# Kernel tuning notes

Measured on AMD Instinct MI355X. Metric: run time of the kernel, lower is better.

## Reference

```python
import jax, jax.numpy as jnp
import numpy as np

IN_DIM, OUT_DIM, N_PROTO, RANK = 1024, 1024, 32, 16


def setup_inputs() -> dict:
    key = jax.random.key(0)
    ks = jax.random.split(key, 5)
    x = jax.random.normal(ks[0], (2, 4096, IN_DIM), dtype=jnp.float32)
    prototypes = jax.random.normal(ks[1], (N_PROTO, IN_DIM), dtype=jnp.float32) * 0.02
    B = jax.random.normal(ks[2], (N_PROTO, RANK, IN_DIM), dtype=jnp.float32) * 0.02
    A = jax.random.normal(ks[3], (N_PROTO, OUT_DIM, RANK), dtype=jnp.float32) * 0.02
    bias = jnp.zeros((N_PROTO, OUT_DIM), dtype=jnp.float32)
    temp = jnp.asarray(1.0, dtype=jnp.float32)
    return {"x": x, "prototypes": prototypes, "B": B, "A": A, "bias": bias, "temp": temp}


def reference(x, prototypes, B, A, bias, temp):
    lead = x.shape[:-1]
    xf = x.reshape(-1, IN_DIM)                       # [N, in]
    x2 = jnp.sum(xf * xf, axis=1, keepdims=True)     # [N,1]
    p2 = jnp.sum(prototypes * prototypes, axis=1)    # [P]
    d2 = x2 + p2[None, :] - 2.0 * (xf @ prototypes.T)
    dists = jnp.sqrt(jnp.maximum(d2, 0.0))           # [N,P]
    t = jnp.maximum(jnp.abs(temp), 0.1)
    w = jax.nn.softmax(-dists / t, axis=1)           # [N,P]
    topw, topi = jax.lax.top_k(w, 2)                 # [N,2]
    topw = topw / jnp.sum(topw, axis=1, keepdims=True)
    out = jnp.zeros((xf.shape[0], OUT_DIM), dtype=xf.dtype)
    for tslot in range(2):
        idx = topi[:, tslot]                          # [N]
        wt = topw[:, tslot:tslot + 1]                 # [N,1]
        h = jnp.einsum('nri,ni->nr', B[idx], xf)      # gathered low-rank down-proj
        y = jnp.einsum('nor,nr->no', A[idx], h) + bias[idx]
        out = out + wt * y
    return out.reshape(*lead, OUT_DIM)
```

## Files before the change

kernel.cpp:

```cpp
#include <hip/hip_runtime.h>
#include <math.h>

#define ROWS_TOTAL 8192
#define KDIM 1024
#define NPROTO 32
#define RNK 16
#define OUTD 1024
#define TIE_EPS 1.30e-4
#define DELTA 4.0e-5f
#define FLAG_CAP 4096

__global__ __launch_bounds__(256) void prep_kernel(
    const float* __restrict__ A, const float* __restrict__ B,
    const float* __restrict__ proto, float* __restrict__ At,
    float* __restrict__ Bt, float* __restrict__ Pt, double* __restrict__ p2g,
    int* __restrict__ counts, int* __restrict__ flagcnt)
{
    __shared__ float T[16 * 68];
    __shared__ float U[64 * 20];
    __shared__ double red[32][9];
    __shared__ float TP[32][33];
    const int tid = threadIdx.x;

    if (blockIdx.x < 128) {
        const int p = blockIdx.x >> 2;
        const int c0 = (blockIdx.x & 3) * 4;
        const float4* B4 = (const float4*)(B + (size_t)p * RNK * KDIM);
        const float4* A4 = (const float4*)(A + (size_t)p * OUTD * RNK);
        float4* Bt4 = (float4*)(Bt + (size_t)p * KDIM * RNK);
        float4* At4 = (float4*)(At + (size_t)p * RNK * OUTD);
        for (int c = c0; c < c0 + 4; ++c) {
            {
                int r = tid >> 4, kk = tid & 15;
                float4 v = B4[r * 256 + c * 16 + kk];
                *(float4*)&T[r * 68 + kk * 4] = v;
            }
            {
                int o = tid >> 2, rq = tid & 3;
                float4 v = A4[(c * 64 + o) * 4 + rq];
                *(float4*)&U[o * 20 + rq * 4] = v;
            }
            __syncthreads();
            {
                int k = tid >> 2, rq = tid & 3;
                float4 g = make_float4(T[(rq * 4 + 0) * 68 + k], T[(rq * 4 + 1) * 68 + k],
                                       T[(rq * 4 + 2) * 68 + k], T[(rq * 4 + 3) * 68 + k]);
                Bt4[(c * 64 + k) * 4 + rq] = g;
            }
            {
                int r = tid >> 4, ow = tid & 15;
                float4 g = make_float4(U[(ow * 4 + 0) * 20 + r], U[(ow * 4 + 1) * 20 + r],
                                       U[(ow * 4 + 2) * 20 + r], U[(ow * 4 + 3) * 20 + r]);
                At4[r * 256 + c * 16 + ow] = g;
            }
            __syncthreads();
        }
    } else {
        const int qb = blockIdx.x - 128;
        if (qb == 0) {
            if (tid < 64) counts[tid] = 0;
            if (tid == 64) flagcnt[0] = 0;
            {
                const int p = tid >> 3, seg = tid & 7;
                const float* a = proto + (size_t)p * KDIM + seg * 128;
                double s = 0.0;
                for (int k = 0; k < 128; ++k) {
                    double v = (double)a[k];
                    s = fma(v, v, s);
                }
                red[p][seg] = s;
            }
            __syncthreads();
            if (tid < 32) {
                double acc = red[tid][0];
                #pragma unroll
                for (int j = 1; j < 8; ++j) acc += red[tid][j];
                p2g[tid] = acc;
            }
        }
        float4* Pt4 = (float4*)Pt;
        for (int kc = qb * 8; kc < qb * 8 + 8; ++kc) {
            {
                int cc = tid >> 3, kk4 = tid & 7;
                float4 v = *(const float4*)(proto + (size_t)cc * KDIM + kc * 32 + kk4 * 4);
                TP[cc][kk4 * 4 + 0] = v.x; TP[cc][kk4 * 4 + 1] = v.y;
                TP[cc][kk4 * 4 + 2] = v.z; TP[cc][kk4 * 4 + 3] = v.w;
            }
            __syncthreads();
            {
                int kk = tid >> 3, c4 = tid & 7;
                float4 g = make_float4(TP[c4 * 4 + 0][kk], TP[c4 * 4 + 1][kk],
                                       TP[c4 * 4 + 2][kk], TP[c4 * 4 + 3][kk]);
                Pt4[(kc * 32 + kk) * 8 + c4] = g;
            }
            __syncthreads();
        }
    }
}

#define INS(kb, ib) { \
    bool lt1 = (kb) < k1, lt2 = (kb) < k2, lt3 = (kb) < k3, lt4 = (kb) < k4; \
    float nk4 = lt3 ? k3 : (lt4 ? (kb) : k4); int ni4 = lt3 ? i3 : (lt4 ? (ib) : i4); \
    float nk3 = lt2 ? k2 : (lt3 ? (kb) : k3); int ni3 = lt2 ? i2 : (lt3 ? (ib) : i3); \
    float nk2 = lt1 ? k1 : (lt2 ? (kb) : k2); int ni2 = lt1 ? i1 : (lt2 ? (ib) : i2); \
    k4 = nk4; i4 = ni4; k3 = nk3; i3 = ni3; k2 = nk2; i2 = ni2; \
    if (lt1) { k1 = (kb); i1 = (ib); } }

__global__ __launch_bounds__(256) void route_kernel(
    const float* __restrict__ x, const float* __restrict__ Pt,
    const float* __restrict__ temp, const double* __restrict__ p2g,
    float4* __restrict__ route, int* __restrict__ counts,
    int* __restrict__ flagcnt, int* __restrict__ flaglist)
{
    __shared__ float Xs[8 * KDIM];
    __shared__ float part[4][8][33];
    __shared__ float x2p[4][8];
    __shared__ int lcnt[64];

    const int tid = threadIdx.x;
    const int w = tid >> 6, l = tid & 63;
    const int c4 = l & 7, kslot = l >> 3;
    const int rowbase = blockIdx.x * 8;

    if (tid < 64) lcnt[tid] = 0;

    const float4* x4 = (const float4*)x;
    float sq[8];
    #pragma unroll
    for (int j = 0; j < 8; ++j) {
        float4 v = x4[(size_t)rowbase * 256 + j * 256 + tid];
        ((float4*)Xs)[j * 256 + tid] = v;
        sq[j] = fmaf(v.x, v.x, fmaf(v.y, v.y, fmaf(v.z, v.z, v.w * v.w)));
    }
    #pragma unroll
    for (int m = 1; m < 64; m <<= 1) {
        #pragma unroll
        for (int j = 0; j < 8; ++j) sq[j] += __shfl_xor(sq[j], m);
    }
    if (l == 0) {
        #pragma unroll
        for (int j = 0; j < 8; ++j) x2p[w][j] = sq[j];
    }
    __syncthreads();

    float acc[8][4];
    #pragma unroll
    for (int j = 0; j < 8; ++j)
        #pragma unroll
        for (int jj = 0; jj < 4; ++jj) acc[j][jj] = 0.f;

    const float4* Pt4 = (const float4*)Pt;
    const int kbase = w * 256;
    #pragma unroll 4
    for (int i = 0; i < 32; ++i) {
        const int k = kbase + i * 8 + kslot;
        float4 pv = Pt4[k * 8 + c4];
        #pragma unroll
        for (int j = 0; j < 8; ++j) {
            float xv = Xs[j * KDIM + k];
            acc[j][0] = fmaf(xv, pv.x, acc[j][0]);
            acc[j][1] = fmaf(xv, pv.y, acc[j][1]);
            acc[j][2] = fmaf(xv, pv.z, acc[j][2]);
            acc[j][3] = fmaf(xv, pv.w, acc[j][3]);
        }
    }
    #pragma unroll
    for (int m = 8; m < 64; m <<= 1) {
        #pragma unroll
        for (int j = 0; j < 8; ++j) {
            acc[j][0] += __shfl_xor(acc[j][0], m);
            acc[j][1] += __shfl_xor(acc[j][1], m);
            acc[j][2] += __shfl_xor(acc[j][2], m);
            acc[j][3] += __shfl_xor(acc[j][3], m);
        }
    }
    if (kslot == 0) {
        #pragma unroll
        for (int j = 0; j < 8; ++j) {
            part[w][j][4 * c4 + 0] = acc[j][0];
            part[w][j][4 * c4 + 1] = acc[j][1];
            part[w][j][4 * c4 + 2] = acc[j][2];
            part[w][j][4 * c4 + 3] = acc[j][3];
        }
    }
    __syncthreads();

    {
        const int rowsel = tid >> 5, c = tid & 31;
        float dsum = (part[0][rowsel][c] + part[1][rowsel][c])
                   + (part[2][rowsel][c] + part[3][rowsel][c]);
        float key = (float)(p2g[c] - 2.0 * (double)dsum);
        float x2 = (x2p[0][rowsel] + x2p[1][rowsel])
                 + (x2p[2][rowsel] + x2p[3][rowsel]);

        float k1 = key, k2 = 3.0e38f, k3 = 3.1e38f, k4 = 3.2e38f;
        int i1 = c, i2 = 64, i3 = 65, i4 = 66;
        #pragma unroll
        for (int m = 1; m < 32; m <<= 1) {
            float b1 = __shfl_xor(k1, m), b2 = __shfl_xor(k2, m);
            float b3 = __shfl_xor(k3, m), b4 = __shfl_xor(k4, m);
            int j1 = __shfl_xor(i1, m), j2 = __shfl_xor(i2, m);
            int j3 = __shfl_xor(i3, m), j4 = __shfl_xor(i4, m);
            INS(b1, j1); INS(b2, j2); INS(b3, j3); INS(b4, j4);
        }
        if (c == 0) {
            const int row = rowbase + rowsel;
            const float tf = fmaxf(fabsf(temp[0]), 0.1f);
            bool amb = (k2 - k1 < DELTA) || (k3 - k2 < DELTA)
                    || (fabsf((k3 - k2) - (float)TIE_EPS) < DELTA)
                    || (k4 - k3 < DELTA);
            bool tie = (k3 - k2) < (float)TIE_EPS;
            bool take3 = tie && (i3 < i2);
            float ksel = take3 ? k3 : k2;
            int   isel = take3 ? i3 : i2;
            float d0 = sqrtf(fmaxf(x2 + k1, 0.f));
            float d1 = sqrtf(fmaxf(x2 + ksel, 0.f));
            float e = expf((d0 - d1) / tf);
            float w0 = 1.f / (1.f + e);
            route[row] = make_float4(__int_as_float(i1), __int_as_float(isel),
                                     w0, e * w0);
            atomicAdd(&lcnt[i1], 1);
            atomicAdd(&lcnt[32 + isel], 1);
            if (amb) {
                int fi = atomicAdd(flagcnt, 1);
                if (fi < FLAG_CAP) flaglist[fi] = row;
            }
        }
    }
    __syncthreads();
    if (tid < 64) atomicAdd(&counts[tid], lcnt[tid]);
}

__global__ __launch_bounds__(256) void refine_scan_kernel(
    const float* __restrict__ x, const float* __restrict__ proto,
    const float* __restrict__ temp, const double* __restrict__ p2g,
    float4* __restrict__ route, int* __restrict__ counts,
    const int* __restrict__ flagcnt, const int* __restrict__ flaglist,
    int2* __restrict__ segs)
{
    const int tid = threadIdx.x;
    const int w = tid >> 6, l = tid & 63;
    const int c = l & 31, half = l >> 5;
    const int n = min(flagcnt[0], FLAG_CAP);

    for (int f = w; f < n; f += 4) {
        const int row = flaglist[f];
        const float* xr = x + (size_t)row * KDIM;
        double xs = 0.0;
        for (int k = l * 16; k < l * 16 + 16; ++k) {
            double v = (double)xr[k];
            xs = fma(v, v, xs);
        }
        #pragma unroll
        for (int m = 1; m < 64; m <<= 1) xs += __shfl_xor(xs, m);
        const float* pr = proto + (size_t)c * KDIM + half * 512;
        const float* xh = xr + half * 512;
        double d0a = 0.0, d1a = 0.0;
        for (int k = 0; k < 512; k += 2) {
            d0a = fma((double)xh[k], (double)pr[k], d0a);
            d1a = fma((double)xh[k + 1], (double)pr[k + 1], d1a);
        }
        double acc = d0a + d1a;
        acc += __shfl_xor(acc, 32);
        double key = p2g[c] - 2.0 * acc;

        double k1 = key, k2 = 1.0e300, k3 = 1.1e300;
        int i1 = c, i2 = 64, i3 = 65;
        #pragma unroll
        for (int m = 1; m < 32; m <<= 1) {
            double b1 = __shfl_xor(k1, m), b2 = __shfl_xor(k2, m), b3 = __shfl_xor(k3, m);
            int j1 = __shfl_xor(i1, m), j2 = __shfl_xor(i2, m), j3 = __shfl_xor(i3, m);
            bool c1 = (k1 < b1) || (k1 == b1 && i1 < j1);
            double m1 = c1 ? k1 : b1, M1 = c1 ? b1 : k1;
            int mi1 = c1 ? i1 : j1, Mi1 = c1 ? j1 : i1;
            bool c2 = (k2 < b2) || (k2 == b2 && i2 < j2);
            double m2 = c2 ? k2 : b2;
            int mi2 = c2 ? i2 : j2;
            bool c3 = (k3 < b3) || (k3 == b3 && i3 < j3);
            double m3 = c3 ? k3 : b3;
            int mi3 = c3 ? i3 : j3;
            bool c4 = (M1 < m2) || (M1 == m2 && Mi1 < mi2);
            double t2 = c4 ? M1 : m2, T2 = c4 ? m2 : M1;
            int ti2 = c4 ? Mi1 : mi2, Ti2 = c4 ? mi2 : Mi1;
            bool c5 = (T2 < m3) || (T2 == m3 && Ti2 < mi3);
            k1 = m1; i1 = mi1;
            k2 = t2; i2 = ti2;
            k3 = c5 ? T2 : m3; i3 = c5 ? Ti2 : mi3;
        }
        if (l == 0) {
            const double tmp = (double)fmaxf(fabsf(temp[0]), 0.1f);
            bool tie = (k3 - k2) < TIE_EPS;
            bool take3 = tie && (i3 < i2);
            double ksel = take3 ? k3 : k2;
            int isel = take3 ? i3 : i2;
            double dd0 = sqrt(fmax(xs + k1, 0.0));
            double dd1 = sqrt(fmax(xs + ksel, 0.0));
            float e = expf((float)((dd0 - dd1) / tmp));
            float w0 = 1.f / (1.f + e);
            float4 old = route[row];
            int oi1 = __float_as_int(old.x), oisel = __float_as_int(old.y);
            if (oi1 != i1) { atomicAdd(&counts[oi1], -1); atomicAdd(&counts[i1], 1); }
            if (oisel != isel) { atomicAdd(&counts[32 + oisel], -1); atomicAdd(&counts[32 + isel], 1); }
            route[row] = make_float4(__int_as_float(i1), __int_as_float(isel),
                                     w0, e * w0);
        }
    }
    __syncthreads();
    if (tid < 64) {
        int v = atomicAdd(&counts[tid], 0);
        int sum = v;
        #pragma unroll
        for (int off = 1; off < 32; off <<= 1) {
            int u = __shfl_up(sum, off, 32);
            if ((tid & 31) >= off) sum += u;
        }
        counts[tid] = sum - v;
        segs[tid] = make_int2(sum - v, sum);
    }
}

__global__ __launch_bounds__(256) void scatter_kernel(
    const float4* __restrict__ route, int* __restrict__ counts,
    int* __restrict__ rowlist0, int* __restrict__ rowlist1)
{
    __shared__ int lcnt[64];
    __shared__ int gbase[64];
    const int tid = threadIdx.x;
    const int i = blockIdx.x * 256 + tid;
    if (tid < 64) lcnt[tid] = 0;
    __syncthreads();
    float4 rt = route[i];
    int p0 = __float_as_int(rt.x);
    int p1 = __float_as_int(rt.y);
    int lp0 = atomicAdd(&lcnt[p0], 1);
    int lp1 = atomicAdd(&lcnt[32 + p1], 1);
    __syncthreads();
    if (tid < 64) gbase[tid] = atomicAdd(&counts[tid], lcnt[tid]);
    __syncthreads();
    rowlist0[gbase[p0] + lp0] = i;
    rowlist1[gbase[32 + p1] + lp1] = i;
}

__global__ __launch_bounds__(256) void h_kernel(
    const float* __restrict__ x, const float* __restrict__ Bt,
    const int* __restrict__ rowlist0, const int* __restrict__ rowlist1,
    const int2* __restrict__ segs, float* __restrict__ hws)
{
    __shared__ float part[4][4][17];
    __shared__ int xoffs[4];

    const int tid = threadIdx.x;
    const int w = tid >> 6, l = tid & 63;
    const int kq = l >> 2, rq = l & 3;
    const int s = blockIdx.y;
    const int slot = s >> 5;
    const int2 sg = segs[s];
    const int* rl = slot ? rowlist1 : rowlist0;
    const float4* Btp = (const float4*)(Bt + (size_t)(s & 31) * KDIM * RNK);
    const int qbase = w * 256;

    for (int c = blockIdx.x; ; c += gridDim.x) {
        const int base = sg.x + c * 4;
        if (base >= sg.y) break;
        const int m = min(4, sg.y - base);

        if (tid < 4) xoffs[tid] = rl[base + min(tid, m - 1)] * KDIM;
        __syncthreads();
        const int x0 = xoffs[0], x1 = xoffs[1], x2 = xoffs[2], x3 = xoffs[3];

        float4 a0 = {0,0,0,0}, a1 = {0,0,0,0}, a2 = {0,0,0,0}, a3 = {0,0,0,0};
        #pragma unroll
        for (int i = 0; i < 16; ++i) {
            const int k = qbase + i * 16 + kq;
            float4 bv = Btp[k * 4 + rq];
            float v0 = x[x0 + k], v1 = x[x1 + k], v2 = x[x2 + k], v3 = x[x3 + k];
            a0.x = fmaf(v0, bv.x, a0.x); a0.y = fmaf(v0, bv.y, a0.y);
            a0.z = fmaf(v0, bv.z, a0.z); a0.w = fmaf(v0, bv.w, a0.w);
            a1.x = fmaf(v1, bv.x, a1.x); a1.y = fmaf(v1, bv.y, a1.y);
            a1.z = fmaf(v1, bv.z, a1.z); a1.w = fmaf(v1, bv.w, a1.w);
            a2.x = fmaf(v2, bv.x, a2.x); a2.y = fmaf(v2, bv.y, a2.y);
            a2.z = fmaf(v2, bv.z, a2.z); a2.w = fmaf(v2, bv.w, a2.w);
            a3.x = fmaf(v3, bv.x, a3.x); a3.y = fmaf(v3, bv.y, a3.y);
            a3.z = fmaf(v3, bv.z, a3.z); a3.w = fmaf(v3, bv.w, a3.w);
        }
        #pragma unroll
        for (int msk = 4; msk < 64; msk <<= 1) {
            a0.x += __shfl_xor(a0.x, msk); a0.y += __shfl_xor(a0.y, msk);
            a0.z += __shfl_xor(a0.z, msk); a0.w += __shfl_xor(a0.w, msk);
            a1.x += __shfl_xor(a1.x, msk); a1.y += __shfl_xor(a1.y, msk);
            a1.z += __shfl_xor(a1.z, msk); a1.w += __shfl_xor(a1.w, msk);
            a2.x += __shfl_xor(a2.x, msk); a2.y += __shfl_xor(a2.y, msk);
            a2.z += __shfl_xor(a2.z, msk); a2.w += __shfl_xor(a2.w, msk);
            a3.x += __shfl_xor(a3.x, msk); a3.y += __shfl_xor(a3.y, msk);
            a3.z += __shfl_xor(a3.z, msk); a3.w += __shfl_xor(a3.w, msk);
        }
        if (kq == 0) {
            *(float4*)&part[w][0][rq * 4] = a0;
            *(float4*)&part[w][1][rq * 4] = a1;
            *(float4*)&part[w][2][rq * 4] = a2;
            *(float4*)&part[w][3][rq * 4] = a3;
        }
        __syncthreads();
        if (tid < 64) {
            const int e = tid >> 4, r = tid & 15;
            if (e < m) {
                float hsum = (part[0][e][r] + part[1][e][r])
                           + (part[2][e][r] + part[3][e][r]);
                hws[(size_t)(slot * ROWS_TOTAL + base + e) * 16 + r] = hsum;
            }
        }
        __syncthreads();
    }
}

__global__ __launch_bounds__(256) void y_kernel(
    const float* __restrict__ At, const float* __restrict__ bias,
    const float4* __restrict__ route, const int* __restrict__ rowlist,
    const int2* __restrict__ segs, const float* __restrict__ hws,
    float* __restrict__ out, int slot)
{
    __shared__ float hsm[16][17];
    __shared__ int rows[16];
    __shared__ float wts[16];

    const int tid = threadIdx.x;
    const int f4 = tid;
    const int p = blockIdx.y;
    const int2 sg = segs[slot * 32 + p];
    const float4* Atp = (const float4*)(At + (size_t)p * RNK * OUTD);
    const float4 bb = ((const float4*)(bias + (size_t)p * OUTD))[f4];

    float4 Areg[16];
    #pragma unroll
    for (int r = 0; r < 16; ++r) Areg[r] = Atp[r * 256 + f4];

    for (int c = blockIdx.x; ; c += gridDim.x) {
        const int base = sg.x + c * 16;
        if (base >= sg.y) break;
        const int m = min(16, sg.y - base);
        const int gbase = slot * ROWS_TOTAL + base;

        if (tid < 16) {
            int rr = rowlist[base + min(tid, m - 1)];
            rows[tid] = rr;
            float4 rt = route[rr];
            wts[tid] = slot ? rt.w : rt.z;
        }
        {
            const int e = tid >> 4, r = tid & 15;
            hsm[e][r] = hws[(size_t)(gbase + min(e, m - 1)) * 16 + r];
        }
        __syncthreads();

        for (int e = 0; e < m; ++e) {
            float4 acc = bb;
            #pragma unroll
            for (int r = 0; r < 16; ++r) {
                float hr = hsm[e][r];
                acc.x = fmaf(hr, Areg[r].x, acc.x);
                acc.y = fmaf(hr, Areg[r].y, acc.y);
                acc.z = fmaf(hr, Areg[r].z, acc.z);
                acc.w = fmaf(hr, Areg[r].w, acc.w);
            }
            const float w = wts[e];
            float4 v = make_float4(w * acc.x, w * acc.y, w * acc.z, w * acc.w);
            float4* dst = (float4*)(out + (size_t)rows[e] * OUTD) + f4;
            if (slot) {
                float4 old = *dst;
                v.x += old.x; v.y += old.y; v.z += old.z; v.w += old.w;
            }
            *dst = v;
        }
        __syncthreads();
    }
}

extern "C" void kernel_launch(void* const* d_in, const int* in_sizes, int n_in,
                              void* d_out, int out_size, void* d_ws, size_t ws_size,
                              hipStream_t stream) {
    const float* x     = (const float*)d_in[0];
    const float* proto = (const float*)d_in[1];
    const float* B     = (const float*)d_in[2];
    const float* A     = (const float*)d_in[3];
    const float* bias  = (const float*)d_in[4];
    const float* temp  = (const float*)d_in[5];
    float* out = (float*)d_out;

    char* wsb = (char*)d_ws;
    float4* route = (float4*)wsb;
    int* rowlist0 = (int*)(wsb + 131072);
    int* rowlist1 = rowlist0 + ROWS_TOTAL;
    int* counts   = (int*)(wsb + 196608);
    int2* segs    = (int2*)(wsb + 196864);
    double* p2g   = (double*)(wsb + 197376);
    int* flagcnt  = (int*)(wsb + 197632);
    int* flaglist = (int*)(wsb + 197760);
    float* Pt     = (float*)(wsb + 262144);
    float* Bt     = (float*)(wsb + 393216);
    float* At     = (float*)(wsb + 393216 + 2097152);
    float* hws    = (float*)(wsb + 393216 + 2 * 2097152);

    prep_kernel<<<132, 256, 0, stream>>>(A, B, proto, At, Bt, Pt, p2g,
                                         counts, flagcnt);
    route_kernel<<<ROWS_TOTAL / 8, 256, 0, stream>>>(x, Pt, temp, p2g, route,
                                                     counts, flagcnt, flaglist);
    refine_scan_kernel<<<1, 256, 0, stream>>>(x, proto, temp, p2g, route,
                                              counts, flagcnt, flaglist, segs);
    scatter_kernel<<<ROWS_TOTAL / 256, 256, 0, stream>>>(route, counts, rowlist0, rowlist1);
    h_kernel<<<dim3(64, 64), 256, 0, stream>>>(x, Bt, rowlist0, rowlist1, segs, hws);
    y_kernel<<<dim3(16, NPROTO), 256, 0, stream>>>(At, bias, route, rowlist0, segs, hws, out, 0);
    y_kernel<<<dim3(16, NPROTO), 256, 0, stream>>>(At, bias, route, rowlist1, segs, hws, out, 1);
}
```

Before: 152.8 us.

## Compute low-rank down-projection per row tile with x staged in shared memory

The h_kernel switches from per-prototype segments of gathered rows to contiguous 8-row tiles. Each tile is loaded into LDS once and both top-2 slots are computed from it, and hws is now indexed by the original row. This makes x reads coalesced and removes the double gather of x across the two slots. The cost is that Bt reads now depend on each row's prototype and are strided by 16 floats, so they are scattered across the wave. The y_kernel is updated to index hws by row id, which adds an extra block barrier.

```diff
diff --git a/kernel.cpp b/kernel.cpp
--- a/kernel.cpp
+++ b/kernel.cpp
@@ -343,74 +343,40 @@
 
 __global__ __launch_bounds__(256) void h_kernel(
     const float* __restrict__ x, const float* __restrict__ Bt,
-    const int* __restrict__ rowlist0, const int* __restrict__ rowlist1,
-    const int2* __restrict__ segs, float* __restrict__ hws)
-{
-    __shared__ float part[4][4][17];
-    __shared__ int xoffs[4];
-
-    const int tid = threadIdx.x;
-    const int w = tid >> 6, l = tid & 63;
-    const int kq = l >> 2, rq = l & 3;
-    const int s = blockIdx.y;
-    const int slot = s >> 5;
-    const int2 sg = segs[s];
-    const int* rl = slot ? rowlist1 : rowlist0;
-    const float4* Btp = (const float4*)(Bt + (size_t)(s & 31) * KDIM * RNK);
-    const int qbase = w * 256;
-
-    for (int c = blockIdx.x; ; c += gridDim.x) {
-        const int base = sg.x + c * 4;
-        if (base >= sg.y) break;
-        const int m = min(4, sg.y - base);
-
-        if (tid < 4) xoffs[tid] = rl[base + min(tid, m - 1)] * KDIM;
-        __syncthreads();
-        const int x0 = xoffs[0], x1 = xoffs[1], x2 = xoffs[2], x3 = xoffs[3];
-
-        float4 a0 = {0,0,0,0}, a1 = {0,0,0,0}, a2 = {0,0,0,0}, a3 = {0,0,0,0};
-        #pragma unroll
-        for (int i = 0; i < 16; ++i) {
-            const int k = qbase + i * 16 + kq;
-            float4 bv = Btp[k * 4 + rq];
-            float v0 = x[x0 + k], v1 = x[x1 + k], v2 = x[x2 + k], v3 = x[x3 + k];
-            a0.x = fmaf(v0, bv.x, a0.x); a0.y = fmaf(v0, bv.y, a0.y);
-            a0.z = fmaf(v0, bv.z, a0.z); a0.w = fmaf(v0, bv.w, a0.w);
-            a1.x = fmaf(v1, bv.x, a1.x); a1.y = fmaf(v1, bv.y, a1.y);
-            a1.z = fmaf(v1, bv.z, a1.z); a1.w = fmaf(v1, bv.w, a1.w);
-            a2.x = fmaf(v2, bv.x, a2.x); a2.y = fmaf(v2, bv.y, a2.y);
-            a2.z = fmaf(v2, bv.z, a2.z); a2.w = fmaf(v2, bv.w, a2.w);
-            a3.x = fmaf(v3, bv.x, a3.x); a3.y = fmaf(v3, bv.y, a3.y);
-            a3.z = fmaf(v3, bv.z, a3.z); a3.w = fmaf(v3, bv.w, a3.w);
-        }
-        #pragma unroll
-        for (int msk = 4; msk < 64; msk <<= 1) {
-            a0.x += __shfl_xor(a0.x, msk); a0.y += __shfl_xor(a0.y, msk);
-            a0.z += __shfl_xor(a0.z, msk); a0.w += __shfl_xor(a0.w, msk);
-            a1.x += __shfl_xor(a1.x, msk); a1.y += __shfl_xor(a1.y, msk);
-            a1.z += __shfl_xor(a1.z, msk); a1.w += __shfl_xor(a1.w, msk);
-            a2.x += __shfl_xor(a2.x, msk); a2.y += __shfl_xor(a2.y, msk);
-            a2.z += __shfl_xor(a2.z, msk); a2.w += __shfl_xor(a2.w, msk);
-            a3.x += __shfl_xor(a3.x, msk); a3.y += __shfl_xor(a3.y, msk);
-            a3.z += __shfl_xor(a3.z, msk); a3.w += __shfl_xor(a3.w, msk);
-        }
-        if (kq == 0) {
-            *(float4*)&part[w][0][rq * 4] = a0;
-            *(float4*)&part[w][1][rq * 4] = a1;
-            *(float4*)&part[w][2][rq * 4] = a2;
-            *(float4*)&part[w][3][rq * 4] = a3;
-        }
-        __syncthreads();
-        if (tid < 64) {
-            const int e = tid >> 4, r = tid & 15;
-            if (e < m) {
-                float hsum = (part[0][e][r] + part[1][e][r])
-                           + (part[2][e][r] + part[3][e][r]);
-                hws[(size_t)(slot * ROWS_TOTAL + base + e) * 16 + r] = hsum;
-            }
-        }
-        __syncthreads();
-    }
+    const float4* __restrict__ route, float* __restrict__ hws)
+{
+    __shared__ float Xs[8 * KDIM];
+    __shared__ int ps[16];
+
+    const int tid = threadIdx.x;
+    const int rowbase = blockIdx.x * 8;
+
+    const float4* x4 = (const float4*)x;
+    #pragma unroll
+    for (int j = 0; j < 8; ++j)
+        ((float4*)Xs)[j * 256 + tid] = x4[(size_t)rowbase * 256 + j * 256 + tid];
+    if (tid < 16) {
+        float4 rt = route[rowbase + (tid >> 1)];
+        ps[tid] = __float_as_int((tid & 1) ? rt.y : rt.x);
+    }
+    __syncthreads();
+
+    const int pair = tid >> 4, rank = tid & 15;
+    const int rrow = pair >> 1, slot = pair & 1;
+    const float* Bp = Bt + (size_t)ps[pair] * KDIM * RNK + rank;
+    const float* Xr = &Xs[rrow * KDIM];
+
+    float a0 = 0.f, a1 = 0.f, a2 = 0.f, a3 = 0.f;
+    #pragma unroll 8
+    for (int i = 0; i < 256; ++i) {
+        const int k = i * 4;
+        a0 = fmaf(Xr[k + 0], Bp[(k + 0) * 16], a0);
+        a1 = fmaf(Xr[k + 1], Bp[(k + 1) * 16], a1);
+        a2 = fmaf(Xr[k + 2], Bp[(k + 2) * 16], a2);
+        a3 = fmaf(Xr[k + 3], Bp[(k + 3) * 16], a3);
+    }
+    hws[(size_t)(slot * ROWS_TOTAL + rowbase + rrow) * 16 + rank] =
+        (a0 + a1) + (a2 + a3);
 }
 
 __global__ __launch_bounds__(256) void y_kernel(
@@ -438,7 +404,6 @@
         const int base = sg.x + c * 16;
         if (base >= sg.y) break;
         const int m = min(16, sg.y - base);
-        const int gbase = slot * ROWS_TOTAL + base;
 
         if (tid < 16) {
             int rr = rowlist[base + min(tid, m - 1)];
@@ -446,9 +411,10 @@
             float4 rt = route[rr];
             wts[tid] = slot ? rt.w : rt.z;
         }
+        __syncthreads();
         {
             const int e = tid >> 4, r = tid & 15;
-            hsm[e][r] = hws[(size_t)(gbase + min(e, m - 1)) * 16 + r];
+            hsm[e][r] = hws[(size_t)(slot * ROWS_TOTAL + rows[e]) * 16 + r];
         }
         __syncthreads();
 
@@ -507,7 +473,7 @@
     refine_scan_kernel<<<1, 256, 0, stream>>>(x, proto, temp, p2g, route,
                                               counts, flagcnt, flaglist, segs);
     scatter_kernel<<<ROWS_TOTAL / 256, 256, 0, stream>>>(route, counts, rowlist0, rowlist1);
-    h_kernel<<<dim3(64, 64), 256, 0, stream>>>(x, Bt, rowlist0, rowlist1, segs, hws);
+    h_kernel<<<ROWS_TOTAL / 8, 256, 0, stream>>>(x, Bt, route, hws);
     y_kernel<<<dim3(16, NPROTO), 256, 0, stream>>>(At, bias, route, rowlist0, segs, hws, out, 0);
     y_kernel<<<dim3(16, NPROTO), 256, 0, stream>>>(At, bias, route, rowlist1, segs, hws, out, 1);
 }
```

Result: slower. 156.2 us (+2.2%).

## Stage eight gathered x rows in LDS per h_kernel tile and index hws by row

Applied to the files above, without the earlier changes.

The h_kernel now processes 8 rows per iteration instead of 4. It stages the gathered x rows into shared memory with coalesced float4 loads, then reuses each Bt float4 across all 8 rows, which cuts redundant Bt traffic and replaces scattered scalar x loads. The hws layout changes from segment-position indexing to original-row indexing, and y_kernel gains a barrier so it can read rows from shared memory. The grid x-dimension is halved. The trade-offs are a 32KB LDS allocation, which may lower occupancy, and more accumulator registers.

```diff
diff --git a/kernel.cpp b/kernel.cpp
--- a/kernel.cpp
+++ b/kernel.cpp
@@ -346,67 +346,75 @@
     const int* __restrict__ rowlist0, const int* __restrict__ rowlist1,
     const int2* __restrict__ segs, float* __restrict__ hws)
 {
-    __shared__ float part[4][4][17];
-    __shared__ int xoffs[4];
+    __shared__ __align__(16) float Xs[8 * KDIM];
+    __shared__ float part[4][8][16];
+    __shared__ int rows[8];
 
     const int tid = threadIdx.x;
-    const int w = tid >> 6, l = tid & 63;
-    const int kq = l >> 2, rq = l & 3;
     const int s = blockIdx.y;
     const int slot = s >> 5;
     const int2 sg = segs[s];
     const int* rl = slot ? rowlist1 : rowlist0;
     const float4* Btp = (const float4*)(Bt + (size_t)(s & 31) * KDIM * RNK);
-    const int qbase = w * 256;
+
+    const int k64 = tid >> 2;
+    const int r4 = tid & 3;
+    const int w = tid >> 6;
+    const int l = tid & 63;
 
     for (int c = blockIdx.x; ; c += gridDim.x) {
-        const int base = sg.x + c * 4;
+        const int base = sg.x + c * 8;
         if (base >= sg.y) break;
-        const int m = min(4, sg.y - base);
-
-        if (tid < 4) xoffs[tid] = rl[base + min(tid, m - 1)] * KDIM;
-        __syncthreads();
-        const int x0 = xoffs[0], x1 = xoffs[1], x2 = xoffs[2], x3 = xoffs[3];
-
-        float4 a0 = {0,0,0,0}, a1 = {0,0,0,0}, a2 = {0,0,0,0}, a3 = {0,0,0,0};
-        #pragma unroll
+        const int m = min(8, sg.y - base);
+
+        if (tid < 8) rows[tid] = rl[base + min(tid, m - 1)];
+        __syncthreads();
+
+        const float4* x4 = (const float4*)x;
+        #pragma unroll
+        for (int j = 0; j < 8; ++j)
+            ((float4*)Xs)[j * 256 + tid] = x4[(size_t)rows[j] * 256 + tid];
+        __syncthreads();
+
+        float4 a[8];
+        #pragma unroll
+        for (int e = 0; e < 8; ++e) a[e] = make_float4(0.f, 0.f, 0.f, 0.f);
+
+        #pragma unroll 4
         for (int i = 0; i < 16; ++i) {
-            const int k = qbase + i * 16 + kq;
-            float4 bv = Btp[k * 4 + rq];
-            float v0 = x[x0 + k], v1 = x[x1 + k], v2 = x[x2 + k], v3 = x[x3 + k];
-            a0.x = fmaf(v0, bv.x, a0.x); a0.y = fmaf(v0, bv.y, a0.y);
-            a0.z = fmaf(v0, bv.z, a0.z); a0.w = fmaf(v0, bv.w, a0.w);
-            a1.x = fmaf(v1, bv.x, a1.x); a1.y = fmaf(v1, bv.y, a1.y);
-            a1.z = fmaf(v1, bv.z, a1.z); a1.w = fmaf(v1, bv.w, a1.w);
-            a2.x = fmaf(v2, bv.x, a2.x); a2.y = fmaf(v2, bv.y, a2.y);
-            a2.z = fmaf(v2, bv.z, a2.z); a2.w = fmaf(v2, bv.w, a2.w);
-            a3.x = fmaf(v3, bv.x, a3.x); a3.y = fmaf(v3, bv.y, a3.y);
-            a3.z = fmaf(v3, bv.z, a3.z); a3.w = fmaf(v3, bv.w, a3.w);
+            const int k = i * 64 + k64;
+            float4 bv = Btp[k * 4 + r4];
+            #pragma unroll
+            for (int e = 0; e < 8; ++e) {
+                float xv = Xs[e * KDIM + k];
+                a[e].x = fmaf(xv, bv.x, a[e].x);
+                a[e].y = fmaf(xv, bv.y, a[e].y);
+                a[e].z = fmaf(xv, bv.z, a[e].z);
+                a[e].w = fmaf(xv, bv.w, a[e].w);
+            }
         }
         #pragma unroll
         for (int msk = 4; msk < 64; msk <<= 1) {
-            a0.x += __shfl_xor(a0.x, msk); a0.y += __shfl_xor(a0.y, msk);
-            a0.z += __shfl_xor(a0.z, msk); a0.w += __shfl_xor(a0.w, msk);
-            a1.x += __shfl_xor(a1.x, msk); a1.y += __shfl_xor(a1.y, msk);
-            a1.z += __shfl_xor(a1.z, msk); a1.w += __shfl_xor(a1.w, msk);
-            a2.x += __shfl_xor(a2.x, msk); a2.y += __shfl_xor(a2.y, msk);
-            a2.z += __shfl_xor(a2.z, msk); a2.w += __shfl_xor(a2.w, msk);
-            a3.x += __shfl_xor(a3.x, msk); a3.y += __shfl_xor(a3.y, msk);
-            a3.z += __shfl_xor(a3.z, msk); a3.w += __shfl_xor(a3.w, msk);
-        }
-        if (kq == 0) {
-            *(float4*)&part[w][0][rq * 4] = a0;
-            *(float4*)&part[w][1][rq * 4] = a1;
-            *(float4*)&part[w][2][rq * 4] = a2;
-            *(float4*)&part[w][3][rq * 4] = a3;
-        }
-        __syncthreads();
-        if (tid < 64) {
+            #pragma unroll
+            for (int e = 0; e < 8; ++e) {
+                a[e].x += __shfl_xor(a[e].x, msk);
+                a[e].y += __shfl_xor(a[e].y, msk);
+                a[e].z += __shfl_xor(a[e].z, msk);
+                a[e].w += __shfl_xor(a[e].w, msk);
+            }
+        }
+        if (l < 4) {
+            #pragma unroll
+            for (int e = 0; e < 8; ++e)
+                *(float4*)&part[w][e][l * 4] = a[e];
+        }
+        __syncthreads();
+        if (tid < 128) {
             const int e = tid >> 4, r = tid & 15;
             if (e < m) {
                 float hsum = (part[0][e][r] + part[1][e][r])
                            + (part[2][e][r] + part[3][e][r]);
-                hws[(size_t)(slot * ROWS_TOTAL + base + e) * 16 + r] = hsum;
+                hws[(size_t)(slot * ROWS_TOTAL + rows[e]) * 16 + r] = hsum;
             }
         }
         __syncthreads();
@@ -438,7 +446,6 @@
         const int base = sg.x + c * 16;
         if (base >= sg.y) break;
         const int m = min(16, sg.y - base);
-        const int gbase = slot * ROWS_TOTAL + base;
 
         if (tid < 16) {
             int rr = rowlist[base + min(tid, m - 1)];
@@ -446,9 +453,10 @@
             float4 rt = route[rr];
             wts[tid] = slot ? rt.w : rt.z;
         }
+        __syncthreads();
         {
             const int e = tid >> 4, r = tid & 15;
-            hsm[e][r] = hws[(size_t)(gbase + min(e, m - 1)) * 16 + r];
+            hsm[e][r] = hws[(size_t)(slot * ROWS_TOTAL + rows[e]) * 16 + r];
         }
         __syncthreads();
 
@@ -507,7 +515,7 @@
     refine_scan_kernel<<<1, 256, 0, stream>>>(x, proto, temp, p2g, route,
                                               counts, flagcnt, flaglist, segs);
     scatter_kernel<<<ROWS_TOTAL / 256, 256, 0, stream>>>(route, counts, rowlist0, rowlist1);
-    h_kernel<<<dim3(64, 64), 256, 0, stream>>>(x, Bt, rowlist0, rowlist1, segs, hws);
+    h_kernel<<<dim3(32, 64), 256, 0, stream>>>(x, Bt, rowlist0, rowlist1, segs, hws);
     y_kernel<<<dim3(16, NPROTO), 256, 0, stream>>>(At, bias, route, rowlist0, segs, hws, out, 0);
     y_kernel<<<dim3(16, NPROTO), 256, 0, stream>>>(At, bias, route, rowlist1, segs, hws, out, 1);
 }
```

Result: slower. 157.8 us (+3.3%).
